# Kernel optimization log

Measured on AMD Instinct MI355X. Metric: run time of the kernel, lower is better.

## Reference

```python
import jax, jax.numpy as jnp
import numpy as np

D = 1024      # n_embd
H = 16        # n_head
HD = D // H   # head_size = 64


def _layernorm(x, g, b, eps=1e-5):
    mu = jnp.mean(x, axis=-1, keepdims=True)
    var = jnp.mean((x - mu) ** 2, axis=-1, keepdims=True)
    return (x - mu) * jax.lax.rsqrt(var + eps) * g + b


def setup_inputs() -> dict:
    key = jax.random.key(0)
    ks = jax.random.split(key, 12)
    s = lambda fan_in: 1.0 / np.sqrt(fan_in)
    inp = {
        "x": jax.random.normal(ks[0], (4, 2048, D), dtype=jnp.float32),
        # attention projections (bias=False in Head), per-head weights fused into [D, D]
        "wq": jax.random.uniform(ks[1], (D, D), jnp.float32, -s(D), s(D)),
        "wk": jax.random.uniform(ks[2], (D, D), jnp.float32, -s(D), s(D)),
        "wv": jax.random.uniform(ks[3], (D, D), jnp.float32, -s(D), s(D)),
        "wo": jax.random.uniform(ks[4], (D, D), jnp.float32, -s(D), s(D)),
        "bo": jax.random.uniform(ks[5], (D,), jnp.float32, -s(D), s(D)),
        # feed-forward: D -> 4D -> D
        "w1": jax.random.uniform(ks[6], (D, 4 * D), jnp.float32, -s(D), s(D)),
        "b1": jax.random.uniform(ks[7], (4 * D,), jnp.float32, -s(D), s(D)),
        "w2": jax.random.uniform(ks[8], (4 * D, D), jnp.float32, -s(4 * D), s(4 * D)),
        "b2": jax.random.uniform(ks[9], (D,), jnp.float32, -s(4 * D), s(4 * D)),
        # layernorms
        "g_ln1": jnp.ones((D,), jnp.float32),
        "b_ln1": jnp.zeros((D,), jnp.float32),
        "g_ln2": jnp.ones((D,), jnp.float32),
        "b_ln2": jnp.zeros((D,), jnp.float32),
    }
    return inp


def reference(x, wq, wk, wv, wo, bo, w1, b1, w2, b2, g_ln1, b_ln1, g_ln2, b_ln2):
    B, T, _ = x.shape
    # --- self-attention on ln1(x) ---
    h = _layernorm(x, g_ln1, b_ln1)
    q = (h @ wq).reshape(B, T, H, HD)
    k = (h @ wk).reshape(B, T, H, HD)
    v = (h @ wv).reshape(B, T, H, HD)
    scores = jnp.einsum("bqhd,bkhd->bhqk", q, k) * (HD ** -0.5)
    causal = jnp.tril(jnp.ones((T, T), dtype=bool))
    scores = jnp.where(causal, scores, -jnp.inf)
    wei = jax.nn.softmax(scores, axis=-1)                    # [B,H,T,T]
    attn = jnp.einsum("bhqk,bkhd->bqhd", wei, v).reshape(B, T, D)
    x = x + attn @ wo + bo
    # --- feed-forward on ln2(x) ---
    h2 = _layernorm(x, g_ln2, b_ln2)
    x = x + jax.nn.relu(h2 @ w1 + b1) @ w2 + b2
    return x
```

## Files before the change

### kernel.cpp

```cpp
#include <hip/hip_runtime.h>
#include <cstdint>

typedef __bf16 bf16x8 __attribute__((ext_vector_type(8)));
typedef float f32x4 __attribute__((ext_vector_type(4)));
typedef unsigned int u32x4 __attribute__((ext_vector_type(4)));
typedef unsigned int u32x2 __attribute__((ext_vector_type(2)));
typedef unsigned short u16x4 __attribute__((ext_vector_type(4)));

#define D_MODEL 1024
#define SEQ     2048
#define NBATCH  4
#define NHEAD   16
#define HDIM    64
#define NTOK    (NBATCH * SEQ)
#define QSCALE  0.18033688011112042f

__device__ __forceinline__ unsigned short f2bf(float f) {
  unsigned int u = __builtin_bit_cast(unsigned int, f);
  u += 0x7FFFu + ((u >> 16) & 1u);
  return (unsigned short)(u >> 16);
}

__device__ __forceinline__ float bf2f(unsigned short s) {
  return __builtin_bit_cast(float, (unsigned int)s << 16);
// ... 55 lines not shown
                                                 const float* __restrict__ bb,
                                                 unsigned short* __restrict__ out) {
  const int row = blockIdx.x, tid = threadIdx.x;
  float4 xv;
  if (FPIN) {
    xv = ((const float4*)((const float*)xin + (size_t)row * D_MODEL))[tid];
  } else {
    const u16x4 bv4 = ((const u16x4*)((const unsigned short*)xin + (size_t)row * D_MODEL))[tid];
    xv.x = bf2f(bv4.x); xv.y = bf2f(bv4.y); xv.z = bf2f(bv4.z); xv.w = bf2f(bv4.w);
  }
  float s  = xv.x + xv.y + xv.z + xv.w;
  float ss = xv.x * xv.x + xv.y * xv.y + xv.z * xv.z + xv.w * xv.w;
  #pragma unroll
  for (int off = 1; off < 64; off <<= 1) { s += __shfl_xor(s, off); ss += __shfl_xor(ss, off); }
  __shared__ float red[8];
  const int wave = tid >> 6, lane = tid & 63;
  if (lane == 0) { red[wave] = s; red[4 + wave] = ss; }
  __syncthreads();
  s  = red[0] + red[1] + red[2] + red[3];
  ss = red[4] + red[5] + red[6] + red[7];
  const float mu   = s * (1.0f / D_MODEL);
  const float var  = ss * (1.0f / D_MODEL) - mu * mu;
  const float rstd = rsqrtf(var + 1e-5f);
  const float4 gv = ((const float4*)g)[tid];
  const float4 bv = ((const float4*)bb)[tid];
  u16x4 o;
  o.x = f2bf((xv.x - mu) * rstd * gv.x + bv.x);
  o.y = f2bf((xv.y - mu) * rstd * gv.y + bv.y);
  o.z = f2bf((xv.z - mu) * rstd * gv.z + bv.z);
  o.w = f2bf((xv.w - mu) * rstd * gv.w + bv.w);
  *(u16x4*)(out + (size_t)row * D_MODEL + tid * 4) = o;
}

template <bool BIAS, bool RELU, int RES, bool OBF, bool QKV>
__global__ __launch_bounds__(256) void gemm_bt(const unsigned short* __restrict__ A,
                                               const unsigned short* __restrict__ Bt,
                                               const float* __restrict__ bias,
                                               const void* __restrict__ res,
                                               void* __restrict__ out,
                                               unsigned short* __restrict__ qb,
                                               unsigned short* __restrict__ kp,
                                               unsigned short* __restrict__ vt,
                                               int M, int N, int K) {
  __shared__ __align__(16) unsigned short As[128 * 64];
  __shared__ __align__(16) unsigned short Bs[128 * 64];
  const int tid  = threadIdx.x;
  const int lin = blockIdx.y * gridDim.x + blockIdx.x;
  const int xcd = lin & 7, idx = lin >> 3;
  const int by = xcd * 8 + (idx & 7);
  const int bx = idx >> 3;
  const int row0 = by * 128, col0 = bx * 128;
  const int wave = tid >> 6, lane = tid & 63;
  const int wm = wave >> 1, wn = wave & 1;
  const int l15 = lane & 15, quad = lane >> 4;
  f32x4 acc[4][4] = {};

  const int tr = tid >> 3;
  const int tc = (tid & 7) ^ (tr & 7);
  const unsigned short* gA = A  + (size_t)(row0 + tr) * K + tc * 8;
  const unsigned short* gB = Bt + (size_t)(col0 + tr) * K + tc * 8;

  const int rowA = (wm * 64 + l15) * 64;
  const int rowB = (wn * 64 + l15) * 64;
  const int swz0 = (quad ^ (l15 & 7)) * 8;
  const int swz1 = ((4 + quad) ^ (l15 & 7)) * 8;

  for (int k0 = 0; k0 < K; k0 += 64) {
    #pragma unroll
    for (int i = 0; i < 4; ++i) {
      gload16(gA + (size_t)(i * 32) * K + k0, As + (i * 256 + tid) * 8);
      gload16(gB + (size_t)(i * 32) * K + k0, Bs + (i * 256 + tid) * 8);
    }
    __syncthreads();
    #pragma unroll
    for (int kf = 0; kf < 2; ++kf) {
      const int swz = kf ? swz1 : swz0;
      bf16x8 af[4], bfr[4];
      #pragma unroll
      for (int t = 0; t < 4; ++t) {
        af[t]  = load8bf(As + rowA + t * 1024 + swz);
        bfr[t] = load8bf(Bs + rowB + t * 1024 + swz);
      }
      #pragma unroll
      for (int i = 0; i < 4; ++i)
        #pragma unroll
        for (int j = 0; j < 4; ++j)
          acc[i][j] = mfma16(af[i], bfr[j], acc[i][j]);
    }
    __syncthreads();
  }

  const size_t rbase = (size_t)row0 + wm * 64 + quad * 4;
  const int cbase = col0 + wn * 64 + l15;
  if (QKV) {
    const int sec = col0 >> 10;
    #pragma unroll
    for (int i = 0; i < 4; ++i) {
      #pragma unroll
      for (int j = 0; j < 4; ++j) {
        const int col = cbase + j * 16;
        if (sec == 0) {
          #pragma unroll
          for (int r = 0; r < 4; ++r) {
            const size_t row = rbase + i * 16 + r;
            qb[row * 1024 + col] = f2bf(acc[i][j][r] * QSCALE);
          }
        } else if (sec == 1) {
          const int c2 = col - 1024, hh = c2 >> 6, d = c2 & 63;
          #pragma unroll
          for (int r = 0; r < 4; ++r) {
            const size_t row = rbase + i * 16 + r;
            const int bb = (int)(row >> 11), t = (int)(row & 2047);
            kp[(((size_t)(bb * 16 + hh)) * SEQ + t) * 64 + d] = f2bf(acc[i][j][r]);
          }
        } else {
          const int c2 = col - 2048, hh = c2 >> 6, d = c2 & 63;
          const size_t t0 = rbase + i * 16;
          const int bb = (int)(t0 >> 11);
          u16x4 pk;
          #pragma unroll
          for (int r = 0; r < 4; ++r) pk[r] = f2bf(acc[i][j][r]);
          *(u16x4*)(vt + ((size_t)(bb * 16 + hh) * 64 + d) * SEQ + (t0 & 2047)) = pk;
        }
      }
    }
  } else {
    #pragma unroll
    for (int i = 0; i < 4; ++i) {
      #pragma unroll
      for (int j = 0; j < 4; ++j) {
        const int col = cbase + j * 16;
        const float bval = BIAS ? bias[col] : 0.0f;
        #pragma unroll
        for (int r = 0; r < 4; ++r) {
          const size_t row = rbase + i * 16 + r;
          float v = acc[i][j][r];
          if (BIAS) v += bval;
          if (RELU) v = fmaxf(v, 0.0f);
          if (RES == 1) v += ((const float*)res)[row * N + col];
          if (RES == 2) v += bf2f(((const unsigned short*)res)[row * N + col]);
          if (OBF)  ((unsigned short*)out)[row * N + col] = f2bf(v);
          else      ((float*)out)[row * N + col] = v;
        }
      }
    }
  }
}

__device__ __forceinline__ void stage_half_512(const unsigned short* __restrict__ src,
                                               unsigned short* dst, int K, int k0,
                                               int h, int tid) {
  #pragma unroll
  for (int l = 0; l < 2; ++l) {
    const int cid = l * 512 + tid;
    const int r = cid >> 3, p = cid & 7, c = p ^ (r & 7);
    gload16(src + (size_t)(h * 128 + r) * K + k0 + c * 8, dst + h * 8192 + cid * 8);
  }
}

template <bool BIAS, bool RELU, int RES, bool OBF, bool QKV>
__global__ __launch_bounds__(512, 2) void gemm256(const unsigned short* __restrict__ A,
                                                  const unsigned short* __restrict__ Bt,
                                                  const float* __restrict__ bias,
                                                  const void* __restrict__ res,
                                                  void* __restrict__ out,
                                                  unsigned short* __restrict__ qb,
                                                  unsigned short* __restrict__ kp,
                                                  unsigned short* __restrict__ vt,
                                                  int M, int N, int K) {
  __shared__ __align__(16) unsigned short lds[2][32768];
  const int tid = threadIdx.x;
  const int lin = blockIdx.y * gridDim.x + blockIdx.x;
  const int xcd = lin & 7, idx = lin >> 3;
  const int by = xcd * 4 + (idx & 3);
  const int bx = idx >> 2;
  const int row0 = by * 256, col0 = bx * 256;
  const int wave = tid >> 6, lane = tid & 63;
  const int wm = wave >> 2, wn = wave & 3;
  const int l15 = lane & 15, quad = lane >> 4;
  const int swz0 = (quad ^ (l15 & 7)) * 8;
  const int swz1 = ((4 + quad) ^ (l15 & 7)) * 8;

  const unsigned short* gA = A  + (size_t)row0 * K;
  const unsigned short* gB = Bt + (size_t)col0 * K;

  unsigned short* As0 = &lds[0][0];
  unsigned short* Bs0 = &lds[0][16384];
  unsigned short* As1 = &lds[1][0];
  unsigned short* Bs1 = &lds[1][16384];

  f32x4 acc[8][4] = {};
  const int KT = K >> 6;

  stage_half_512(gA, As0, K, 0, 0, tid);
  stage_half_512(gA, As0, K, 0, 1, tid);
  stage_half_512(gB, Bs0, K, 0, 0, tid);
  stage_half_512(gB, Bs0, K, 0, 1, tid);
  stage_half_512(gB, Bs1, K, 64, 0, tid);
  stage_half_512(gB, Bs1, K, 64, 1, tid);
  asm volatile("s_waitcnt vmcnt(4)" ::: "memory");
  asm volatile("s_barrier" ::: "memory");

  for (int t = 0; t < KT; ++t) {
    unsigned short* As  = (t & 1) ? As1 : As0;
    unsigned short* Bs  = (t & 1) ? Bs1 : Bs0;
    unsigned short* Asn = (t & 1) ? As0 : As1;
    const int k1 = (t + 1) << 6, k2 = (t + 2) << 6;
    bf16x8 a0[2][4], b01[2][2], b23[2][2];

    #pragma unroll
    for (int i = 0; i < 4; ++i) {
      const unsigned short* ap = As + (wm * 128 + i * 16 + l15) * 64;
      a0[0][i] = load8bf(ap + swz0);
      a0[1][i] = load8bf(ap + swz1);
    }
    #pragma unroll
    for (int j = 0; j < 2; ++j) {
      const unsigned short* bp = Bs + (wn * 64 + j * 16 + l15) * 64;
      b01[0][j] = load8bf(bp + swz0);
      b01[1][j] = load8bf(bp + swz1);
    }
    if (t + 1 < KT) stage_half_512(gA, Asn, K, k1, 0, tid);
    asm volatile("s_barrier" ::: "memory");
    __builtin_amdgcn_s_setprio(1);
    #pragma unroll
    for (int kf = 0; kf < 2; ++kf)
      #pragma unroll
      for (int i = 0; i < 4; ++i)
        #pragma unroll
        for (int j = 0; j < 2; ++j)
          acc[i][j] = mfma16(a0[kf][i], b01[kf][j], acc[i][j]);
    __builtin_amdgcn_s_setprio(0);
    asm volatile("s_barrier" ::: "memory");

    #pragma unroll
    for (int j = 0; j < 2; ++j) {
      const unsigned short* bp = Bs + (wn * 64 + 32 + j * 16 + l15) * 64;
      b23[0][j] = load8bf(bp + swz0);
      b23[1][j] = load8bf(bp + swz1);
    }
    if (t + 1 < KT) stage_half_512(gA, Asn, K, k1, 1, tid);
    asm volatile("s_barrier" ::: "memory");
    __builtin_amdgcn_s_setprio(1);
    #pragma unroll
    for (int kf = 0; kf < 2; ++kf)
      #pragma unroll
      for (int i = 0; i < 4; ++i)
        #pragma unroll
        for (int j = 0; j < 2; ++j)
          acc[i][2 + j] = mfma16(a0[kf][i], b23[kf][j], acc[i][2 + j]);
    __builtin_amdgcn_s_setprio(0);
    asm volatile("s_barrier" ::: "memory");

    #pragma unroll
    for (int i = 0; i < 4; ++i) {
      const unsigned short* ap = As + (wm * 128 + 64 + i * 16 + l15) * 64;
      a0[0][i] = load8bf(ap + swz0);
      a0[1][i] = load8bf(ap + swz1);
    }
    if (t + 2 < KT) stage_half_512(gB, Bs, K, k2, 0, tid);
    asm volatile("s_barrier" ::: "memory");
    __builtin_amdgcn_s_setprio(1);
    #pragma unroll
    for (int kf = 0; kf < 2; ++kf)
      #pragma unroll
      for (int i = 0; i < 4; ++i)
        #pragma unroll
        for (int j = 0; j < 2; ++j)
          acc[4 + i][2 + j] = mfma16(a0[kf][i], b23[kf][j], acc[4 + i][2 + j]);
    __builtin_amdgcn_s_setprio(0);
    asm volatile("s_barrier" ::: "memory");

    if (t + 2 < KT) stage_half_512(gB, Bs, K, k2, 1, tid);
    asm volatile("s_barrier" ::: "memory");
    __builtin_amdgcn_s_setprio(1);
    #pragma unroll
    for (int kf = 0; kf < 2; ++kf)
      #pragma unroll
      for (int i = 0; i < 4; ++i)
        #pragma unroll
        for (int j = 0; j < 2; ++j)
          acc[4 + i][j] = mfma16(a0[kf][i], b01[kf][j], acc[4 + i][j]);
    __builtin_amdgcn_s_setprio(0);
    if (t + 2 < KT) asm volatile("s_waitcnt vmcnt(4)" ::: "memory");
    else            asm volatile("s_waitcnt vmcnt(0)" ::: "memory");
    asm volatile("s_barrier" ::: "memory");
  }

  const size_t rbase = (size_t)row0 + wm * 128 + quad * 4;
  const int cbase = col0 + wn * 64 + l15;
  if (QKV) {
    const int sec = col0 >> 10;
    #pragma unroll
    for (int i = 0; i < 8; ++i) {
      #pragma unroll
      for (int j = 0; j < 4; ++j) {
        const int col = cbase + j * 16;
        if (sec == 0) {
          #pragma unroll
          for (int r = 0; r < 4; ++r) {
            const size_t row = rbase + i * 16 + r;
            qb[row * 1024 + col] = f2bf(acc[i][j][r] * QSCALE);
          }
        } else if (sec == 1) {
          const int c2 = col - 1024, hh = c2 >> 6, d = c2 & 63;
          #pragma unroll
          for (int r = 0; r < 4; ++r) {
            const size_t row = rbase + i * 16 + r;
            const int bb = (int)(row >> 11), tt = (int)(row & 2047);
            kp[(((size_t)(bb * 16 + hh)) * SEQ + tt) * 64 + d] = f2bf(acc[i][j][r]);
          }
        } else {
          const int c2 = col - 2048, hh = c2 >> 6, d = c2 & 63;
          const size_t t0 = rbase + i * 16;
          const int bb = (int)(t0 >> 11);
          u16x4 pk;
          #pragma unroll
          for (int r = 0; r < 4; ++r) pk[r] = f2bf(acc[i][j][r]);
          *(u16x4*)(vt + ((size_t)(bb * 16 + hh) * 64 + d) * SEQ + (t0 & 2047)) = pk;
        }
      }
    }
  } else {
    #pragma unroll
    for (int i = 0; i < 8; ++i) {
      #pragma unroll
      for (int j = 0; j < 4; ++j) {
        const int col = cbase + j * 16;
        const float bval = BIAS ? bias[col] : 0.0f;
        #pragma unroll
        for (int r = 0; r < 4; ++r) {
          const size_t row = rbase + i * 16 + r;
          float v = acc[i][j][r];
          if (BIAS) v += bval;
          if (RELU) v = fmaxf(v, 0.0f);
          if (RES == 1) v += ((const float*)res)[row * N + col];
          if (RES == 2) v += bf2f(((const unsigned short*)res)[row * N + col]);
          if (OBF)  ((unsigned short*)out)[row * N + col] = f2bf(v);
          else      ((float*)out)[row * N + col] = v;
        }
      }
    }
  }
  (void)M;
}

__global__ __launch_bounds__(256) void attn5(const unsigned short* __restrict__ qb,
                                             const unsigned short* __restrict__ kp,
                                             const unsigned short* __restrict__ vt,
                                             unsigned short* __restrict__ attnb) {
  const int lin = (blockIdx.z * 16 + blockIdx.y) * 8 + blockIdx.x;
  const int xcd = lin & 7, idx = lin >> 3;
  const int bh = xcd * 8 + (idx >> 3);
  const int xb = idx & 7;
  const int b = bh >> 4, h = bh & 15;
  const int tid = threadIdx.x, wave = tid >> 6, lane = tid & 63;
  const int l15 = lane & 15, quad = lane >> 4;
  const size_t tokbase = (size_t)b * SEQ;

  __shared__ __align__(16) unsigned short ks[64 * 64];
  __shared__ __align__(16) unsigned short vts[64 * 64];
  __shared__ __align__(16) unsigned short plds[4][32 * 64];

  const unsigned short* kbase = kp + (size_t)bh * SEQ * HDIM;
  const unsigned short* vbase = vt + (size_t)bh * HDIM * SEQ;

  for (int half = 0; half < 2; ++half) {
    const int qblk = (half == 0) ? (15 - xb) : xb;
    const int qw0 = qblk * 128 + wave * 32;

    bf16x8 qf[2][2];
    #pragma unroll
    for (int qfi = 0; qfi < 2; ++qfi)
      #pragma unroll
      for (int kf = 0; kf < 2; ++kf)
        qf[qfi][kf] = load8bf(qb + (tokbase + qw0 + qfi * 16 + l15) * 1024
                              + h * HDIM + kf * 32 + quad * 8);

    f32x4 o[2][4] = {};
// ... 93 lines not shown
                              void* d_out, int out_size, void* d_ws, size_t ws_size,
                              hipStream_t stream) {
  const float* x    = (const float*)d_in[0];
  const float* wq   = (const float*)d_in[1];
  const float* wk   = (const float*)d_in[2];
  const float* wv   = (const float*)d_in[3];
  const float* wo   = (const float*)d_in[4];
  const float* bo   = (const float*)d_in[5];
  const float* w1   = (const float*)d_in[6];
  const float* b1   = (const float*)d_in[7];
  const float* w2   = (const float*)d_in[8];
  const float* b2   = (const float*)d_in[9];
  const float* g1   = (const float*)d_in[10];
  const float* bl1  = (const float*)d_in[11];
  const float* g2   = (const float*)d_in[12];
  const float* bl2  = (const float*)d_in[13];
  float* out = (float*)d_out;

  char* ws = (char*)d_ws;
  size_t off = 0;
  auto alloc = [&](size_t bytes) { char* p = ws + off; off += (bytes + 255) & ~(size_t)255; return p; };
  unsigned short* wqkv_t = (unsigned short*)alloc((size_t)3072 * 1024 * 2);
  unsigned short* wo_t   = (unsigned short*)alloc((size_t)1024 * 1024 * 2);
  unsigned short* w1_t   = (unsigned short*)alloc((size_t)4096 * 1024 * 2);
  unsigned short* w2_t   = (unsigned short*)alloc((size_t)1024 * 4096 * 2);
  unsigned short* h1     = (unsigned short*)alloc((size_t)NTOK * 1024 * 2);
  unsigned short* kpb    = (unsigned short*)alloc((size_t)NTOK * 1024 * 2);
  unsigned short* vtb    = (unsigned short*)alloc((size_t)NTOK * 1024 * 2);
  unsigned short* attnb  = (unsigned short*)alloc((size_t)NTOK * 1024 * 2);
  unsigned short* h2     = (unsigned short*)alloc((size_t)NTOK * 1024 * 2);
  unsigned short* ffn1   = (unsigned short*)alloc((size_t)NTOK * 4096 * 2);
  unsigned short* qb  = attnb;
  unsigned short* x1b = h1;

  tcast_all<<<12288, 256, 0, stream>>>(wq, wk, wv, wo, w1, w2,
                                       wqkv_t, wo_t, w1_t, w2_t);
  ln_kernel<1><<<NTOK, 256, 0, stream>>>(x, g1, bl1, h1);
  gemm256<false, false, 0, true, true><<<dim3(12, 32), 512, 0, stream>>>(
      h1, wqkv_t, nullptr, nullptr, nullptr, qb, kpb, vtb, NTOK, 3072, 1024);
  attn5<<<dim3(SEQ / 256, NHEAD, NBATCH), 256, 0, stream>>>(qb, kpb, vtb, attnb);
  gemm_bt<true, false, 1, true, false><<<dim3(8, 64), 256, 0, stream>>>(
      attnb, wo_t, bo, x, x1b, nullptr, nullptr, nullptr, NTOK, 1024, 1024);
  ln_kernel<0><<<NTOK, 256, 0, stream>>>(x1b, g2, bl2, h2);
  gemm256<true, true, 0, true, false><<<dim3(16, 32), 512, 0, stream>>>(
      h2, w1_t, b1, nullptr, ffn1, nullptr, nullptr, nullptr, NTOK, 4096, 1024);
  gemm256<true, false, 2, false, false><<<dim3(4, 32), 512, 0, stream>>>(
      ffn1, w2_t, b2, x1b, out, nullptr, nullptr, nullptr, NTOK, 1024, 4096);
  (void)in_sizes; (void)n_in; (void)out_size; (void)ws_size;
}
```

Measured before the change: 503.8 us.

## Add 256x128-tile GEMM variant for QKV and FFN2 to raise grid occupancy

Introduces gemm256n, a 256x128 output-tile GEMM with its own double-buffered LDS schedule (A prefetched two k-steps ahead, B one step ahead). It replaces the 256x256 kernel for the QKV projection and the FFN down-projection, doubling the block count (e.g. FFN2 from 128 to 256 blocks) so more of the machine's compute units get work. The QKV-specific epilogue moves into the new kernel and is removed from the older kernels. The trade-off is lower arithmetic intensity per tile and more A-matrix traffic.

Result: faster. 447.7 us (-11.1%).

```diff
diff --git a/kernel.cpp b/kernel.cpp
--- a/kernel.cpp
+++ b/kernel.cpp
@@ -111,15 +111,12 @@
   *(u16x4*)(out + (size_t)row * D_MODEL + tid * 4) = o;
 }
 
-template <bool BIAS, bool RELU, int RES, bool OBF, bool QKV>
+template <bool BIAS, bool RELU, int RES, bool OBF>
 __global__ __launch_bounds__(256) void gemm_bt(const unsigned short* __restrict__ A,
                                                const unsigned short* __restrict__ Bt,
                                                const float* __restrict__ bias,
                                                const void* __restrict__ res,
                                                void* __restrict__ out,
-                                               unsigned short* __restrict__ qb,
-                                               unsigned short* __restrict__ kp,
-                                               unsigned short* __restrict__ vt,
                                                int M, int N, int K) {
   __shared__ __align__(16) unsigned short As[128 * 64];
   __shared__ __align__(16) unsigned short Bs[128 * 64];
@@ -171,56 +168,22 @@
 
   const size_t rbase = (size_t)row0 + wm * 64 + quad * 4;
   const int cbase = col0 + wn * 64 + l15;
-  if (QKV) {
-    const int sec = col0 >> 10;
-    #pragma unroll
-    for (int i = 0; i < 4; ++i) {
-      #pragma unroll
-      for (int j = 0; j < 4; ++j) {
-        const int col = cbase + j * 16;
-        if (sec == 0) {
-          #pragma unroll
-          for (int r = 0; r < 4; ++r) {
-            const size_t row = rbase + i * 16 + r;
-            qb[row * 1024 + col] = f2bf(acc[i][j][r] * QSCALE);
-          }
-        } else if (sec == 1) {
-          const int c2 = col - 1024, hh = c2 >> 6, d = c2 & 63;
-          #pragma unroll
-          for (int r = 0; r < 4; ++r) {
-            const size_t row = rbase + i * 16 + r;
-            const int bb = (int)(row >> 11), t = (int)(row & 2047);
-            kp[(((size_t)(bb * 16 + hh)) * SEQ + t) * 64 + d] = f2bf(acc[i][j][r]);
-          }
-        } else {
-          const int c2 = col - 2048, hh = c2 >> 6, d = c2 & 63;
-          const size_t t0 = rbase + i * 16;
-          const int bb = (int)(t0 >> 11);
-          u16x4 pk;
-          #pragma unroll
-          for (int r = 0; r < 4; ++r) pk[r] = f2bf(acc[i][j][r]);
-          *(u16x4*)(vt + ((size_t)(bb * 16 + hh) * 64 + d) * SEQ + (t0 & 2047)) = pk;
-        }
-      }
-    }
-  } else {
-    #pragma unroll
-    for (int i = 0; i < 4; ++i) {
-      #pragma unroll
-      for (int j = 0; j < 4; ++j) {
-        const int col = cbase + j * 16;
-        const float bval = BIAS ? bias[col] : 0.0f;
-        #pragma unroll
-        for (int r = 0; r < 4; ++r) {
-          const size_t row = rbase + i * 16 + r;
-          float v = acc[i][j][r];
-          if (BIAS) v += bval;
-          if (RELU) v = fmaxf(v, 0.0f);
-          if (RES == 1) v += ((const float*)res)[row * N + col];
-          if (RES == 2) v += bf2f(((const unsigned short*)res)[row * N + col]);
-          if (OBF)  ((unsigned short*)out)[row * N + col] = f2bf(v);
-          else      ((float*)out)[row * N + col] = v;
-        }
+  #pragma unroll
+  for (int i = 0; i < 4; ++i) {
+    #pragma unroll
+    for (int j = 0; j < 4; ++j) {
+      const int col = cbase + j * 16;
+      const float bval = BIAS ? bias[col] : 0.0f;
+      #pragma unroll
+      for (int r = 0; r < 4; ++r) {
+        const size_t row = rbase + i * 16 + r;
+        float v = acc[i][j][r];
+        if (BIAS) v += bval;
+        if (RELU) v = fmaxf(v, 0.0f);
+        if (RES == 1) v += ((const float*)res)[row * N + col];
+        if (RES == 2) v += bf2f(((const unsigned short*)res)[row * N + col]);
+        if (OBF)  ((unsigned short*)out)[row * N + col] = f2bf(v);
+        else      ((float*)out)[row * N + col] = v;
       }
     }
   }
@@ -237,15 +200,12 @@
   }
 }
 
-template <bool BIAS, bool RELU, int RES, bool OBF, bool QKV>
+template <bool BIAS, bool RELU, int RES, bool OBF>
 __global__ __launch_bounds__(512, 2) void gemm256(const unsigned short* __restrict__ A,
                                                   const unsigned short* __restrict__ Bt,
                                                   const float* __restrict__ bias,
                                                   const void* __restrict__ res,
                                                   void* __restrict__ out,
-                                                  unsigned short* __restrict__ qb,
-                                                  unsigned short* __restrict__ kp,
-                                                  unsigned short* __restrict__ vt,
                                                   int M, int N, int K) {
   __shared__ __align__(16) unsigned short lds[2][32768];
   const int tid = threadIdx.x;
@@ -275,9 +235,13 @@
   stage_half_512(gA, As0, K, 0, 1, tid);
   stage_half_512(gB, Bs0, K, 0, 0, tid);
   stage_half_512(gB, Bs0, K, 0, 1, tid);
-  stage_half_512(gB, Bs1, K, 64, 0, tid);
-  stage_half_512(gB, Bs1, K, 64, 1, tid);
-  asm volatile("s_waitcnt vmcnt(4)" ::: "memory");
+  if (KT > 1) {
+    stage_half_512(gB, Bs1, K, 64, 0, tid);
+    stage_half_512(gB, Bs1, K, 64, 1, tid);
+    asm volatile("s_waitcnt vmcnt(4)" ::: "memory");
+  } else {
+    asm volatile("s_waitcnt vmcnt(0)" ::: "memory");
+  }
   asm volatile("s_barrier" ::: "memory");
 
   for (int t = 0; t < KT; ++t) {
@@ -368,10 +332,137 @@
 
   const size_t rbase = (size_t)row0 + wm * 128 + quad * 4;
   const int cbase = col0 + wn * 64 + l15;
+  #pragma unroll
+  for (int i = 0; i < 8; ++i) {
+    #pragma unroll
+    for (int j = 0; j < 4; ++j) {
+      const int col = cbase + j * 16;
+      const float bval = BIAS ? bias[col] : 0.0f;
+      #pragma unroll
+      for (int r = 0; r < 4; ++r) {
+        const size_t row = rbase + i * 16 + r;
+        float v = acc[i][j][r];
+        if (BIAS) v += bval;
+        if (RELU) v = fmaxf(v, 0.0f);
+        if (RES == 1) v += ((const float*)res)[row * N + col];
+        if (RES == 2) v += bf2f(((const unsigned short*)res)[row * N + col]);
+        if (OBF)  ((unsigned short*)out)[row * N + col] = f2bf(v);
+        else      ((float*)out)[row * N + col] = v;
+      }
+    }
+  }
+  (void)M;
+}
+
+template <bool BIAS, bool RELU, int RES, bool OBF, bool QKV>
+__global__ __launch_bounds__(512, 2) void gemm256n(const unsigned short* __restrict__ A,
+                                                   const unsigned short* __restrict__ Bt,
+                                                   const float* __restrict__ bias,
+                                                   const void* __restrict__ res,
+                                                   void* __restrict__ out,
+                                                   unsigned short* __restrict__ qb,
+                                                   unsigned short* __restrict__ kp,
+                                                   unsigned short* __restrict__ vt,
+                                                   int M, int N, int K) {
+  __shared__ __align__(16) unsigned short lds[2][24576];
+  const int tid = threadIdx.x;
+  const int lin = blockIdx.y * gridDim.x + blockIdx.x;
+  const int xcd = lin & 7, idx = lin >> 3;
+  const int by = xcd * 4 + (idx & 3);
+  const int bx = idx >> 2;
+  const int row0 = by * 256, col0 = bx * 128;
+  const int wave = tid >> 6, lane = tid & 63;
+  const int wm = wave >> 1, wn = wave & 1;
+  const int l15 = lane & 15, quad = lane >> 4;
+  const int swz0 = (quad ^ (l15 & 7)) * 8;
+  const int swz1 = ((4 + quad) ^ (l15 & 7)) * 8;
+
+  const unsigned short* gA = A  + (size_t)row0 * K;
+  const unsigned short* gB = Bt + (size_t)col0 * K;
+
+  unsigned short* As0 = &lds[0][0];
+  unsigned short* Bs0 = &lds[0][16384];
+  unsigned short* As1 = &lds[1][0];
+  unsigned short* Bs1 = &lds[1][16384];
+
+  f32x4 acc[4][4] = {};
+  const int KT = K >> 6;
+
+  stage_half_512(gA, As0, K, 0, 0, tid);
+  stage_half_512(gA, As0, K, 0, 1, tid);
+  stage_half_512(gB, Bs0, K, 0, 0, tid);
+  if (KT > 1) {
+    stage_half_512(gA, As1, K, 64, 0, tid);
+    stage_half_512(gA, As1, K, 64, 1, tid);
+    asm volatile("s_waitcnt vmcnt(4)" ::: "memory");
+  } else {
+    asm volatile("s_waitcnt vmcnt(0)" ::: "memory");
+  }
+  asm volatile("s_barrier" ::: "memory");
+
+  for (int t = 0; t < KT; ++t) {
+    unsigned short* As  = (t & 1) ? As1 : As0;
+    unsigned short* Bs  = (t & 1) ? Bs1 : Bs0;
+    unsigned short* Bsn = (t & 1) ? Bs0 : Bs1;
+    const int k1 = (t + 1) << 6, k2 = (t + 2) << 6;
+    bf16x8 a0[2][4], b01[2][2], b23[2][2];
+
+    #pragma unroll
+    for (int i = 0; i < 4; ++i) {
+      const unsigned short* ap = As + (wm * 64 + i * 16 + l15) * 64;
+      a0[0][i] = load8bf(ap + swz0);
+      a0[1][i] = load8bf(ap + swz1);
+    }
+    #pragma unroll
+    for (int j = 0; j < 2; ++j) {
+      const unsigned short* bp = Bs + (wn * 64 + j * 16 + l15) * 64;
+      b01[0][j] = load8bf(bp + swz0);
+      b01[1][j] = load8bf(bp + swz1);
+    }
+    if (t + 1 < KT) stage_half_512(gB, Bsn, K, k1, 0, tid);
+    asm volatile("s_barrier" ::: "memory");
+    __builtin_amdgcn_s_setprio(1);
+    #pragma unroll
+    for (int kf = 0; kf < 2; ++kf)
+      #pragma unroll
+      for (int i = 0; i < 4; ++i)
+        #pragma unroll
+        for (int j = 0; j < 2; ++j)
+          acc[i][j] = mfma16(a0[kf][i], b01[kf][j], acc[i][j]);
+    __builtin_amdgcn_s_setprio(0);
+    asm volatile("s_barrier" ::: "memory");
+
+    #pragma unroll
+    for (int j = 0; j < 2; ++j) {
+      const unsigned short* bp = Bs + (wn * 64 + 32 + j * 16 + l15) * 64;
+      b23[0][j] = load8bf(bp + swz0);
+      b23[1][j] = load8bf(bp + swz1);
+    }
+    if (t + 2 < KT) {
+      stage_half_512(gA, As, K, k2, 0, tid);
+      stage_half_512(gA, As, K, k2, 1, tid);
+    }
+    asm volatile("s_barrier" ::: "memory");
+    __builtin_amdgcn_s_setprio(1);
+    #pragma unroll
+    for (int kf = 0; kf < 2; ++kf)
+      #pragma unroll
+      for (int i = 0; i < 4; ++i)
+        #pragma unroll
+        for (int j = 0; j < 2; ++j)
+          acc[i][2 + j] = mfma16(a0[kf][i], b23[kf][j], acc[i][2 + j]);
+    __builtin_amdgcn_s_setprio(0);
+    if (t + 2 < KT)      asm volatile("s_waitcnt vmcnt(4)" ::: "memory");
+    else if (t + 1 < KT) asm volatile("s_waitcnt vmcnt(0)" ::: "memory");
+    asm volatile("s_barrier" ::: "memory");
+  }
+
+  const size_t rbase = (size_t)row0 + wm * 64 + quad * 4;
+  const int cbase = col0 + wn * 64 + l15;
   if (QKV) {
     const int sec = col0 >> 10;
     #pragma unroll
-    for (int i = 0; i < 8; ++i) {
+    for (int i = 0; i < 4; ++i) {
       #pragma unroll
       for (int j = 0; j < 4; ++j) {
         const int col = cbase + j * 16;
@@ -402,7 +493,7 @@
     }
   } else {
     #pragma unroll
-    for (int i = 0; i < 8; ++i) {
+    for (int i = 0; i < 4; ++i) {
       #pragma unroll
       for (int j = 0; j < 4; ++j) {
         const int col = cbase + j * 16;
@@ -587,15 +678,15 @@
   tcast_all<<<12288, 256, 0, stream>>>(wq, wk, wv, wo, w1, w2,
                                        wqkv_t, wo_t, w1_t, w2_t);
   ln_kernel<1><<<NTOK, 256, 0, stream>>>(x, g1, bl1, h1);
-  gemm256<false, false, 0, true, true><<<dim3(12, 32), 512, 0, stream>>>(
+  gemm256n<false, false, 0, true, true><<<dim3(24, 32), 512, 0, stream>>>(
       h1, wqkv_t, nullptr, nullptr, nullptr, qb, kpb, vtb, NTOK, 3072, 1024);
   attn5<<<dim3(SEQ / 256, NHEAD, NBATCH), 256, 0, stream>>>(qb, kpb, vtb, attnb);
-  gemm_bt<true, false, 1, true, false><<<dim3(8, 64), 256, 0, stream>>>(
-      attnb, wo_t, bo, x, x1b, nullptr, nullptr, nullptr, NTOK, 1024, 1024);
+  gemm_bt<true, false, 1, true><<<dim3(8, 64), 256, 0, stream>>>(
+      attnb, wo_t, bo, x, x1b, NTOK, 1024, 1024);
   ln_kernel<0><<<NTOK, 256, 0, stream>>>(x1b, g2, bl2, h2);
-  gemm256<true, true, 0, true, false><<<dim3(16, 32), 512, 0, stream>>>(
-      h2, w1_t, b1, nullptr, ffn1, nullptr, nullptr, nullptr, NTOK, 4096, 1024);
-  gemm256<true, false, 2, false, false><<<dim3(4, 32), 512, 0, stream>>>(
+  gemm256<true, true, 0, true><<<dim3(16, 32), 512, 0, stream>>>(
+      h2, w1_t, b1, nullptr, ffn1, NTOK, 4096, 1024);
+  gemm256n<true, false, 2, false, false><<<dim3(8, 32), 512, 0, stream>>>(
       ffn1, w2_t, b2, x1b, out, nullptr, nullptr, nullptr, NTOK, 1024, 4096);
   (void)in_sizes; (void)n_in; (void)out_size; (void)ws_size;
 }
```

## Split FFN2 GEMM over K into two halves with separate reduce kernel

Applied to the files above, without the earlier changes.

The FFN down-projection (K=4096, only 128 tiles of 256x256) is split into two K-halves, which doubles the block count to 256 so more CUs have work. Each half writes fp32 partials into a reused workspace region. A new elementwise kernel then sums the partials and adds the bias and bf16 residual. The cost is extra fp32 partial traffic (about 64MB written and read) plus one more launch. It also removes the dead QKV path from gemm_bt and adds lda/ldb parameters so the kernel can address a slice of K.

After: 467.9 us. -7.1%, faster.

```diff
diff --git a/kernel.cpp b/kernel.cpp
--- a/kernel.cpp
+++ b/kernel.cpp
@@ -111,15 +111,12 @@
   *(u16x4*)(out + (size_t)row * D_MODEL + tid * 4) = o;
 }
 
-template <bool BIAS, bool RELU, int RES, bool OBF, bool QKV>
+template <bool BIAS, bool RELU, int RES, bool OBF>
 __global__ __launch_bounds__(256) void gemm_bt(const unsigned short* __restrict__ A,
                                                const unsigned short* __restrict__ Bt,
                                                const float* __restrict__ bias,
                                                const void* __restrict__ res,
                                                void* __restrict__ out,
-                                               unsigned short* __restrict__ qb,
-                                               unsigned short* __restrict__ kp,
-                                               unsigned short* __restrict__ vt,
                                                int M, int N, int K) {
   __shared__ __align__(16) unsigned short As[128 * 64];
   __shared__ __align__(16) unsigned short Bs[128 * 64];
@@ -171,73 +168,39 @@
 
   const size_t rbase = (size_t)row0 + wm * 64 + quad * 4;
   const int cbase = col0 + wn * 64 + l15;
-  if (QKV) {
-    const int sec = col0 >> 10;
-    #pragma unroll
-    for (int i = 0; i < 4; ++i) {
-      #pragma unroll
-      for (int j = 0; j < 4; ++j) {
-        const int col = cbase + j * 16;
-        if (sec == 0) {
-          #pragma unroll
-          for (int r = 0; r < 4; ++r) {
-            const size_t row = rbase + i * 16 + r;
-            qb[row * 1024 + col] = f2bf(acc[i][j][r] * QSCALE);
-          }
-        } else if (sec == 1) {
-          const int c2 = col - 1024, hh = c2 >> 6, d = c2 & 63;
-          #pragma unroll
-          for (int r = 0; r < 4; ++r) {
-            const size_t row = rbase + i * 16 + r;
-            const int bb = (int)(row >> 11), t = (int)(row & 2047);
-            kp[(((size_t)(bb * 16 + hh)) * SEQ + t) * 64 + d] = f2bf(acc[i][j][r]);
-          }
-        } else {
-          const int c2 = col - 2048, hh = c2 >> 6, d = c2 & 63;
-          const size_t t0 = rbase + i * 16;
-          const int bb = (int)(t0 >> 11);
-          u16x4 pk;
-          #pragma unroll
-          for (int r = 0; r < 4; ++r) pk[r] = f2bf(acc[i][j][r]);
-          *(u16x4*)(vt + ((size_t)(bb * 16 + hh) * 64 + d) * SEQ + (t0 & 2047)) = pk;
-        }
-      }
-    }
-  } else {
-    #pragma unroll
-    for (int i = 0; i < 4; ++i) {
-      #pragma unroll
-      for (int j = 0; j < 4; ++j) {
-        const int col = cbase + j * 16;
-        const float bval = BIAS ? bias[col] : 0.0f;
-        #pragma unroll
-        for (int r = 0; r < 4; ++r) {
-          const size_t row = rbase + i * 16 + r;
-          float v = acc[i][j][r];
-          if (BIAS) v += bval;
-          if (RELU) v = fmaxf(v, 0.0f);
-          if (RES == 1) v += ((const float*)res)[row * N + col];
-          if (RES == 2) v += bf2f(((const unsigned short*)res)[row * N + col]);
-          if (OBF)  ((unsigned short*)out)[row * N + col] = f2bf(v);
-          else      ((float*)out)[row * N + col] = v;
-        }
+  #pragma unroll
+  for (int i = 0; i < 4; ++i) {
+    #pragma unroll
+    for (int j = 0; j < 4; ++j) {
+      const int col = cbase + j * 16;
+      const float bval = BIAS ? bias[col] : 0.0f;
+      #pragma unroll
+      for (int r = 0; r < 4; ++r) {
+        const size_t row = rbase + i * 16 + r;
+        float v = acc[i][j][r];
+        if (BIAS) v += bval;
+        if (RELU) v = fmaxf(v, 0.0f);
+        if (RES == 1) v += ((const float*)res)[row * N + col];
+        if (RES == 2) v += bf2f(((const unsigned short*)res)[row * N + col]);
+        if (OBF)  ((unsigned short*)out)[row * N + col] = f2bf(v);
+        else      ((float*)out)[row * N + col] = v;
       }
     }
   }
 }
 
 __device__ __forceinline__ void stage_half_512(const unsigned short* __restrict__ src,
-                                               unsigned short* dst, int K, int k0,
+                                               unsigned short* dst, int ld, int k0,
                                                int h, int tid) {
   #pragma unroll
   for (int l = 0; l < 2; ++l) {
     const int cid = l * 512 + tid;
     const int r = cid >> 3, p = cid & 7, c = p ^ (r & 7);
-    gload16(src + (size_t)(h * 128 + r) * K + k0 + c * 8, dst + h * 8192 + cid * 8);
-  }
-}
-
-template <bool BIAS, bool RELU, int RES, bool OBF, bool QKV>
+    gload16(src + (size_t)(h * 128 + r) * ld + k0 + c * 8, dst + h * 8192 + cid * 8);
+  }
+}
+
+template <bool BIAS, bool RELU, int RES, bool OBF, bool QKV, bool SPLITK>
 __global__ __launch_bounds__(512, 2) void gemm256(const unsigned short* __restrict__ A,
                                                   const unsigned short* __restrict__ Bt,
                                                   const float* __restrict__ bias,
@@ -246,22 +209,25 @@
                                                   unsigned short* __restrict__ qb,
                                                   unsigned short* __restrict__ kp,
                                                   unsigned short* __restrict__ vt,
-                                                  int M, int N, int K) {
+                                                  int M, int N, int K, int lda, int ldb) {
   __shared__ __align__(16) unsigned short lds[2][32768];
   const int tid = threadIdx.x;
   const int lin = blockIdx.y * gridDim.x + blockIdx.x;
   const int xcd = lin & 7, idx = lin >> 3;
   const int by = xcd * 4 + (idx & 3);
-  const int bx = idx >> 2;
+  const int bxr = idx >> 2;
+  const int ks  = SPLITK ? (bxr >> 2) : 0;
+  const int bx  = SPLITK ? (bxr & 3) : bxr;
   const int row0 = by * 256, col0 = bx * 256;
+  const int koff = SPLITK ? ks * K : 0;
   const int wave = tid >> 6, lane = tid & 63;
   const int wm = wave >> 2, wn = wave & 3;
   const int l15 = lane & 15, quad = lane >> 4;
   const int swz0 = (quad ^ (l15 & 7)) * 8;
   const int swz1 = ((4 + quad) ^ (l15 & 7)) * 8;
 
-  const unsigned short* gA = A  + (size_t)row0 * K;
-  const unsigned short* gB = Bt + (size_t)col0 * K;
+  const unsigned short* gA = A  + (size_t)row0 * lda + koff;
+  const unsigned short* gB = Bt + (size_t)col0 * ldb + koff;
 
   unsigned short* As0 = &lds[0][0];
   unsigned short* Bs0 = &lds[0][16384];
@@ -271,13 +237,17 @@
   f32x4 acc[8][4] = {};
   const int KT = K >> 6;
 
-  stage_half_512(gA, As0, K, 0, 0, tid);
-  stage_half_512(gA, As0, K, 0, 1, tid);
-  stage_half_512(gB, Bs0, K, 0, 0, tid);
-  stage_half_512(gB, Bs0, K, 0, 1, tid);
-  stage_half_512(gB, Bs1, K, 64, 0, tid);
-  stage_half_512(gB, Bs1, K, 64, 1, tid);
-  asm volatile("s_waitcnt vmcnt(4)" ::: "memory");
+  stage_half_512(gA, As0, lda, 0, 0, tid);
+  stage_half_512(gA, As0, lda, 0, 1, tid);
+  stage_half_512(gB, Bs0, ldb, 0, 0, tid);
+  stage_half_512(gB, Bs0, ldb, 0, 1, tid);
+  if (KT > 1) {
+    stage_half_512(gB, Bs1, ldb, 64, 0, tid);
+    stage_half_512(gB, Bs1, ldb, 64, 1, tid);
+    asm volatile("s_waitcnt vmcnt(4)" ::: "memory");
+  } else {
+    asm volatile("s_waitcnt vmcnt(0)" ::: "memory");
+  }
   asm volatile("s_barrier" ::: "memory");
 
   for (int t = 0; t < KT; ++t) {
@@ -299,7 +269,7 @@
       b01[0][j] = load8bf(bp + swz0);
       b01[1][j] = load8bf(bp + swz1);
     }
-    if (t + 1 < KT) stage_half_512(gA, Asn, K, k1, 0, tid);
+    if (t + 1 < KT) stage_half_512(gA, Asn, lda, k1, 0, tid);
     asm volatile("s_barrier" ::: "memory");
     __builtin_amdgcn_s_setprio(1);
     #pragma unroll
@@ -318,7 +288,7 @@
       b23[0][j] = load8bf(bp + swz0);
       b23[1][j] = load8bf(bp + swz1);
     }
-    if (t + 1 < KT) stage_half_512(gA, Asn, K, k1, 1, tid);
+    if (t + 1 < KT) stage_half_512(gA, Asn, lda, k1, 1, tid);
     asm volatile("s_barrier" ::: "memory");
     __builtin_amdgcn_s_setprio(1);
     #pragma unroll
@@ -337,7 +307,7 @@
       a0[0][i] = load8bf(ap + swz0);
       a0[1][i] = load8bf(ap + swz1);
     }
-    if (t + 2 < KT) stage_half_512(gB, Bs, K, k2, 0, tid);
+    if (t + 2 < KT) stage_half_512(gB, Bs, ldb, k2, 0, tid);
     asm volatile("s_barrier" ::: "memory");
     __builtin_amdgcn_s_setprio(1);
     #pragma unroll
@@ -350,7 +320,7 @@
     __builtin_amdgcn_s_setprio(0);
     asm volatile("s_barrier" ::: "memory");
 
-    if (t + 2 < KT) stage_half_512(gB, Bs, K, k2, 1, tid);
+    if (t + 2 < KT) stage_half_512(gB, Bs, ldb, k2, 1, tid);
     asm volatile("s_barrier" ::: "memory");
     __builtin_amdgcn_s_setprio(1);
     #pragma unroll
@@ -400,6 +370,20 @@
         }
       }
     }
+  } else if (SPLITK) {
+    float* po = (float*)out + (size_t)ks * M * N;
+    #pragma unroll
+    for (int i = 0; i < 8; ++i) {
+      #pragma unroll
+      for (int j = 0; j < 4; ++j) {
+        const int col = cbase + j * 16;
+        #pragma unroll
+        for (int r = 0; r < 4; ++r) {
+          const size_t row = rbase + i * 16 + r;
+          po[row * N + col] = acc[i][j][r];
+        }
+      }
+    }
   } else {
     #pragma unroll
     for (int i = 0; i < 8; ++i) {
@@ -422,6 +406,24 @@
     }
   }
   (void)M;
+}
+
+__global__ __launch_bounds__(256) void ffn2_reduce(const float* __restrict__ p0,
+                                                   const float* __restrict__ p1,
+                                                   const float* __restrict__ b2,
+                                                   const unsigned short* __restrict__ x1b,
+                                                   float* __restrict__ out) {
+  const size_t i4 = (size_t)blockIdx.x * 256 + threadIdx.x;
+  const float4 a = ((const float4*)p0)[i4];
+  const float4 b = ((const float4*)p1)[i4];
+  const float4 bi = ((const float4*)b2)[i4 & 255];
+  const u16x4 rv = ((const u16x4*)x1b)[i4];
+  float4 o;
+  o.x = a.x + b.x + bi.x + bf2f(rv.x);
+  o.y = a.y + b.y + bi.y + bf2f(rv.y);
+  o.z = a.z + b.z + bi.z + bf2f(rv.z);
+  o.w = a.w + b.w + bi.w + bf2f(rv.w);
+  ((float4*)out)[i4] = o;
 }
 
 __global__ __launch_bounds__(256) void attn5(const unsigned short* __restrict__ qb,
@@ -583,19 +585,23 @@
   unsigned short* ffn1   = (unsigned short*)alloc((size_t)NTOK * 4096 * 2);
   unsigned short* qb  = attnb;
   unsigned short* x1b = h1;
+  float* part = (float*)kpb;
 
   tcast_all<<<12288, 256, 0, stream>>>(wq, wk, wv, wo, w1, w2,
                                        wqkv_t, wo_t, w1_t, w2_t);
   ln_kernel<1><<<NTOK, 256, 0, stream>>>(x, g1, bl1, h1);
-  gemm256<false, false, 0, true, true><<<dim3(12, 32), 512, 0, stream>>>(
-      h1, wqkv_t, nullptr, nullptr, nullptr, qb, kpb, vtb, NTOK, 3072, 1024);
+  gemm256<false, false, 0, true, true, false><<<dim3(12, 32), 512, 0, stream>>>(
+      h1, wqkv_t, nullptr, nullptr, nullptr, qb, kpb, vtb, NTOK, 3072, 1024, 1024, 1024);
   attn5<<<dim3(SEQ / 256, NHEAD, NBATCH), 256, 0, stream>>>(qb, kpb, vtb, attnb);
-  gemm_bt<true, false, 1, true, false><<<dim3(8, 64), 256, 0, stream>>>(
-      attnb, wo_t, bo, x, x1b, nullptr, nullptr, nullptr, NTOK, 1024, 1024);
+  gemm_bt<true, false, 1, true><<<dim3(8, 64), 256, 0, stream>>>(
+      attnb, wo_t, bo, x, x1b, NTOK, 1024, 1024);
   ln_kernel<0><<<NTOK, 256, 0, stream>>>(x1b, g2, bl2, h2);
-  gemm256<true, true, 0, true, false><<<dim3(16, 32), 512, 0, stream>>>(
-      h2, w1_t, b1, nullptr, ffn1, nullptr, nullptr, nullptr, NTOK, 4096, 1024);
-  gemm256<true, false, 2, false, false><<<dim3(4, 32), 512, 0, stream>>>(
-      ffn1, w2_t, b2, x1b, out, nullptr, nullptr, nullptr, NTOK, 1024, 4096);
+  gemm256<true, true, 0, true, false, false><<<dim3(16, 32), 512, 0, stream>>>(
+      h2, w1_t, b1, nullptr, ffn1, nullptr, nullptr, nullptr, NTOK, 4096, 1024, 1024, 1024);
+  gemm256<false, false, 0, false, false, true><<<dim3(8, 32), 512, 0, stream>>>(
+      ffn1, w2_t, nullptr, nullptr, part, nullptr, nullptr, nullptr,
+      NTOK, 1024, 2048, 4096, 4096);
+  ffn2_reduce<<<NTOK * 1024 / 4 / 256, 256, 0, stream>>>(
+      part, part + (size_t)NTOK * 1024, b2, x1b, out);
   (void)in_sizes; (void)n_in; (void)out_size; (void)ws_size;
 }
```

## Add split-K FFN2 GEMM kernel and merge barrier phases in gemm256

Applied to the files above, without the earlier changes.

Adds gemm_ffn2, a dedicated kernel for the second FFN matmul. It uses a 256x128 tile with two wave groups that each own half of K=4096, combines their partial sums through LDS, and launches twice as many blocks (256 instead of 128) so more CUs are busy. gemm256's main loop is also restructured: each half-step stages both LDS halves at once and drops the intermediate barriers, with sched_barrier added to hold instruction order. The QKV epilogue path is removed from gemm_bt. The trade-offs are extra LDS traffic for the split-K reduction and higher register pressure from issuing more loads per phase.

Result: faster. 447.3 us (-11.2%).

```diff
diff --git a/kernel.cpp b/kernel.cpp
--- a/kernel.cpp
+++ b/kernel.cpp
@@ -111,15 +111,12 @@
   *(u16x4*)(out + (size_t)row * D_MODEL + tid * 4) = o;
 }
 
-template <bool BIAS, bool RELU, int RES, bool OBF, bool QKV>
+template <bool BIAS, bool RELU, int RES, bool OBF>
 __global__ __launch_bounds__(256) void gemm_bt(const unsigned short* __restrict__ A,
                                                const unsigned short* __restrict__ Bt,
                                                const float* __restrict__ bias,
                                                const void* __restrict__ res,
                                                void* __restrict__ out,
-                                               unsigned short* __restrict__ qb,
-                                               unsigned short* __restrict__ kp,
-                                               unsigned short* __restrict__ vt,
                                                int M, int N, int K) {
   __shared__ __align__(16) unsigned short As[128 * 64];
   __shared__ __align__(16) unsigned short Bs[128 * 64];
@@ -171,69 +168,35 @@
 
   const size_t rbase = (size_t)row0 + wm * 64 + quad * 4;
   const int cbase = col0 + wn * 64 + l15;
-  if (QKV) {
-    const int sec = col0 >> 10;
-    #pragma unroll
-    for (int i = 0; i < 4; ++i) {
-      #pragma unroll
-      for (int j = 0; j < 4; ++j) {
-        const int col = cbase + j * 16;
-        if (sec == 0) {
-          #pragma unroll
-          for (int r = 0; r < 4; ++r) {
-            const size_t row = rbase + i * 16 + r;
-            qb[row * 1024 + col] = f2bf(acc[i][j][r] * QSCALE);
-          }
-        } else if (sec == 1) {
-          const int c2 = col - 1024, hh = c2 >> 6, d = c2 & 63;
-          #pragma unroll
-          for (int r = 0; r < 4; ++r) {
-            const size_t row = rbase + i * 16 + r;
-            const int bb = (int)(row >> 11), t = (int)(row & 2047);
-            kp[(((size_t)(bb * 16 + hh)) * SEQ + t) * 64 + d] = f2bf(acc[i][j][r]);
-          }
-        } else {
-          const int c2 = col - 2048, hh = c2 >> 6, d = c2 & 63;
-          const size_t t0 = rbase + i * 16;
-          const int bb = (int)(t0 >> 11);
-          u16x4 pk;
-          #pragma unroll
-          for (int r = 0; r < 4; ++r) pk[r] = f2bf(acc[i][j][r]);
-          *(u16x4*)(vt + ((size_t)(bb * 16 + hh) * 64 + d) * SEQ + (t0 & 2047)) = pk;
-        }
-      }
-    }
-  } else {
-    #pragma unroll
-    for (int i = 0; i < 4; ++i) {
-      #pragma unroll
-      for (int j = 0; j < 4; ++j) {
-        const int col = cbase + j * 16;
-        const float bval = BIAS ? bias[col] : 0.0f;
-        #pragma unroll
-        for (int r = 0; r < 4; ++r) {
-          const size_t row = rbase + i * 16 + r;
-          float v = acc[i][j][r];
-          if (BIAS) v += bval;
-          if (RELU) v = fmaxf(v, 0.0f);
-          if (RES == 1) v += ((const float*)res)[row * N + col];
-          if (RES == 2) v += bf2f(((const unsigned short*)res)[row * N + col]);
-          if (OBF)  ((unsigned short*)out)[row * N + col] = f2bf(v);
-          else      ((float*)out)[row * N + col] = v;
-        }
+  #pragma unroll
+  for (int i = 0; i < 4; ++i) {
+    #pragma unroll
+    for (int j = 0; j < 4; ++j) {
+      const int col = cbase + j * 16;
+      const float bval = BIAS ? bias[col] : 0.0f;
+      #pragma unroll
+      for (int r = 0; r < 4; ++r) {
+        const size_t row = rbase + i * 16 + r;
+        float v = acc[i][j][r];
+        if (BIAS) v += bval;
+        if (RELU) v = fmaxf(v, 0.0f);
+        if (RES == 1) v += ((const float*)res)[row * N + col];
+        if (RES == 2) v += bf2f(((const unsigned short*)res)[row * N + col]);
+        if (OBF)  ((unsigned short*)out)[row * N + col] = f2bf(v);
+        else      ((float*)out)[row * N + col] = v;
       }
     }
   }
 }
 
 __device__ __forceinline__ void stage_half_512(const unsigned short* __restrict__ src,
-                                               unsigned short* dst, int K, int k0,
+                                               unsigned short* dst, int ld, int k0,
                                                int h, int tid) {
   #pragma unroll
   for (int l = 0; l < 2; ++l) {
     const int cid = l * 512 + tid;
     const int r = cid >> 3, p = cid & 7, c = p ^ (r & 7);
-    gload16(src + (size_t)(h * 128 + r) * K + k0 + c * 8, dst + h * 8192 + cid * 8);
+    gload16(src + (size_t)(h * 128 + r) * ld + k0 + c * 8, dst + h * 8192 + cid * 8);
   }
 }
 
@@ -275,9 +238,13 @@
   stage_half_512(gA, As0, K, 0, 1, tid);
   stage_half_512(gB, Bs0, K, 0, 0, tid);
   stage_half_512(gB, Bs0, K, 0, 1, tid);
-  stage_half_512(gB, Bs1, K, 64, 0, tid);
-  stage_half_512(gB, Bs1, K, 64, 1, tid);
-  asm volatile("s_waitcnt vmcnt(4)" ::: "memory");
+  if (KT > 1) {
+    stage_half_512(gB, Bs1, K, 64, 0, tid);
+    stage_half_512(gB, Bs1, K, 64, 1, tid);
+    asm volatile("s_waitcnt vmcnt(4)" ::: "memory");
+  } else {
+    asm volatile("s_waitcnt vmcnt(0)" ::: "memory");
+  }
   asm volatile("s_barrier" ::: "memory");
 
   for (int t = 0; t < KT; ++t) {
@@ -298,9 +265,14 @@
       const unsigned short* bp = Bs + (wn * 64 + j * 16 + l15) * 64;
       b01[0][j] = load8bf(bp + swz0);
       b01[1][j] = load8bf(bp + swz1);
-    }
-    if (t + 1 < KT) stage_half_512(gA, Asn, K, k1, 0, tid);
-    asm volatile("s_barrier" ::: "memory");
+      const unsigned short* bp2 = Bs + (wn * 64 + 32 + j * 16 + l15) * 64;
+      b23[0][j] = load8bf(bp2 + swz0);
+      b23[1][j] = load8bf(bp2 + swz1);
+    }
+    if (t + 1 < KT) {
+      stage_half_512(gA, Asn, K, k1, 0, tid);
+      stage_half_512(gA, Asn, K, k1, 1, tid);
+    }
     __builtin_amdgcn_s_setprio(1);
     #pragma unroll
     for (int kf = 0; kf < 2; ++kf)
@@ -309,18 +281,6 @@
         #pragma unroll
         for (int j = 0; j < 2; ++j)
           acc[i][j] = mfma16(a0[kf][i], b01[kf][j], acc[i][j]);
-    __builtin_amdgcn_s_setprio(0);
-    asm volatile("s_barrier" ::: "memory");
-
-    #pragma unroll
-    for (int j = 0; j < 2; ++j) {
-      const unsigned short* bp = Bs + (wn * 64 + 32 + j * 16 + l15) * 64;
-      b23[0][j] = load8bf(bp + swz0);
-      b23[1][j] = load8bf(bp + swz1);
-    }
-    if (t + 1 < KT) stage_half_512(gA, Asn, K, k1, 1, tid);
-    asm volatile("s_barrier" ::: "memory");
-    __builtin_amdgcn_s_setprio(1);
     #pragma unroll
     for (int kf = 0; kf < 2; ++kf)
       #pragma unroll
@@ -329,6 +289,7 @@
         for (int j = 0; j < 2; ++j)
           acc[i][2 + j] = mfma16(a0[kf][i], b23[kf][j], acc[i][2 + j]);
     __builtin_amdgcn_s_setprio(0);
+    __builtin_amdgcn_sched_barrier(0);
     asm volatile("s_barrier" ::: "memory");
 
     #pragma unroll
@@ -337,8 +298,10 @@
       a0[0][i] = load8bf(ap + swz0);
       a0[1][i] = load8bf(ap + swz1);
     }
-    if (t + 2 < KT) stage_half_512(gB, Bs, K, k2, 0, tid);
-    asm volatile("s_barrier" ::: "memory");
+    if (t + 2 < KT) {
+      stage_half_512(gB, Bs, K, k2, 0, tid);
+      stage_half_512(gB, Bs, K, k2, 1, tid);
+    }
     __builtin_amdgcn_s_setprio(1);
     #pragma unroll
     for (int kf = 0; kf < 2; ++kf)
@@ -347,12 +310,6 @@
         #pragma unroll
         for (int j = 0; j < 2; ++j)
           acc[4 + i][2 + j] = mfma16(a0[kf][i], b23[kf][j], acc[4 + i][2 + j]);
-    __builtin_amdgcn_s_setprio(0);
-    asm volatile("s_barrier" ::: "memory");
-
-    if (t + 2 < KT) stage_half_512(gB, Bs, K, k2, 1, tid);
-    asm volatile("s_barrier" ::: "memory");
-    __builtin_amdgcn_s_setprio(1);
     #pragma unroll
     for (int kf = 0; kf < 2; ++kf)
       #pragma unroll
@@ -361,6 +318,7 @@
         for (int j = 0; j < 2; ++j)
           acc[4 + i][j] = mfma16(a0[kf][i], b01[kf][j], acc[4 + i][j]);
     __builtin_amdgcn_s_setprio(0);
+    __builtin_amdgcn_sched_barrier(0);
     if (t + 2 < KT) asm volatile("s_waitcnt vmcnt(4)" ::: "memory");
     else            asm volatile("s_waitcnt vmcnt(0)" ::: "memory");
     asm volatile("s_barrier" ::: "memory");
@@ -424,6 +382,148 @@
   (void)M;
 }
 
+__device__ __forceinline__ void stage32g(const unsigned short* __restrict__ src,
+                                         unsigned short* dst, int ld, int k0,
+                                         int h128, int t256) {
+  #pragma unroll
+  for (int l = 0; l < 2; ++l) {
+    const int cid = l * 256 + t256;
+    const int L = cid >> 3;
+    const int p = cid & 7;
+    const int c = p ^ (L & 7);
+    const int row = h128 * 128 + L * 2 + (c >> 2);
+    gload16(src + (size_t)row * ld + k0 + (c & 3) * 8, dst + h128 * 4096 + cid * 8);
+  }
+}
+
+__device__ __forceinline__ bf16x8 frag32(const unsigned short* tile, int r0,
+                                         int l15, int quad) {
+  const int row = r0 + l15;
+  const int L = row >> 1;
+  const int p = ((row & 1) * 4 + quad) ^ (L & 7);
+  return load8bf(tile + L * 64 + p * 8);
+}
+
+__global__ __launch_bounds__(512, 2) void gemm_ffn2(const unsigned short* __restrict__ A,
+                                                    const unsigned short* __restrict__ Bt,
+                                                    const float* __restrict__ bias,
+                                                    const unsigned short* __restrict__ res,
+                                                    float* __restrict__ out) {
+  __shared__ __align__(16) unsigned short lds[2][2][12288];
+  const int tid = threadIdx.x;
+  const int lin = blockIdx.y * gridDim.x + blockIdx.x;
+  const int xcd = lin & 7, idx = lin >> 3;
+  const int by = xcd * 4 + (idx & 3);
+  const int bx = idx >> 2;
+  const int row0 = by * 256, col0 = bx * 128;
+  const int wave = tid >> 6, lane = tid & 63;
+  const int ks = wave >> 2;
+  const int w4 = wave & 3;
+  const int wm = w4 >> 1, wn = w4 & 1;
+  const int l15 = lane & 15, quad = lane >> 4;
+  const int t256 = tid & 255;
+
+  const unsigned short* gA = A  + (size_t)row0 * 4096 + ks * 2048;
+  const unsigned short* gB = Bt + (size_t)col0 * 4096 + ks * 2048;
+
+  unsigned short* As0 = &lds[ks][0][0];
+  unsigned short* Bs0 = &lds[ks][0][8192];
+  unsigned short* As1 = &lds[ks][1][0];
+  unsigned short* Bs1 = &lds[ks][1][8192];
+
+  f32x4 acc[8][4] = {};
+  const int KT = 64;
+
+  stage32g(gA, As0, 4096, 0, 0, t256);
+  stage32g(gA, As0, 4096, 0, 1, t256);
+  stage32g(gB, Bs0, 4096, 0, 0, t256);
+  stage32g(gB, Bs1, 4096, 32, 0, t256);
+  asm volatile("s_waitcnt vmcnt(2)" ::: "memory");
+  asm volatile("s_barrier" ::: "memory");
+
+  for (int t = 0; t < KT; ++t) {
+    unsigned short* As  = (t & 1) ? As1 : As0;
+    unsigned short* Bs  = (t & 1) ? Bs1 : Bs0;
+    unsigned short* Asn = (t & 1) ? As0 : As1;
+    const int k1 = (t + 1) << 5, k2 = (t + 2) << 5;
+    bf16x8 a[4], b[4];
+
+    #pragma unroll
+    for (int j = 0; j < 4; ++j) b[j] = frag32(Bs, wn * 64 + j * 16, l15, quad);
+    #pragma unroll
+    for (int i = 0; i < 4; ++i) a[i] = frag32(As, wm * 128 + i * 16, l15, quad);
+    if (t + 1 < KT) {
+      stage32g(gA, Asn, 4096, k1, 0, t256);
+      stage32g(gA, Asn, 4096, k1, 1, t256);
+    }
+    __builtin_amdgcn_s_setprio(1);
+    #pragma unroll
+    for (int i = 0; i < 4; ++i)
+      #pragma unroll
+      for (int j = 0; j < 4; ++j)
+        acc[i][j] = mfma16(a[i], b[j], acc[i][j]);
+    __builtin_amdgcn_s_setprio(0);
+    __builtin_amdgcn_sched_barrier(0);
+    asm volatile("s_barrier" ::: "memory");
+
+    #pragma unroll
+    for (int i = 0; i < 4; ++i) a[i] = frag32(As, wm * 128 + 64 + i * 16, l15, quad);
+    if (t + 2 < KT) stage32g(gB, Bs, 4096, k2, 0, t256);
+    __builtin_amdgcn_s_setprio(1);
+    #pragma unroll
+    for (int i = 0; i < 4; ++i)
+      #pragma unroll
+      for (int j = 0; j < 4; ++j)
+        acc[4 + i][j] = mfma16(a[i], b[j], acc[4 + i][j]);
+    __builtin_amdgcn_s_setprio(0);
+    __builtin_amdgcn_sched_barrier(0);
+    if (t + 2 < KT) asm volatile("s_waitcnt vmcnt(2)" ::: "memory");
+    else            asm volatile("s_waitcnt vmcnt(0)" ::: "memory");
+    asm volatile("s_barrier" ::: "memory");
+  }
+
+  float* ex = (float*)&lds[0][0][0];
+  #pragma unroll
+  for (int half = 0; half < 2; ++half) {
+    __syncthreads();
+    if (ks == 1) {
+      #pragma unroll
+      for (int i = 0; i < 4; ++i)
+        #pragma unroll
+        for (int j = 0; j < 4; ++j)
+          *(f32x4*)(ex + ((size_t)(w4 * 16 + i * 4 + j)) * 256 + lane * 4) =
+              acc[half * 4 + i][j];
+    }
+    __syncthreads();
+    if (ks == 0) {
+      #pragma unroll
+      for (int i = 0; i < 4; ++i)
+        #pragma unroll
+        for (int j = 0; j < 4; ++j) {
+          const f32x4 v = *(const f32x4*)(ex + ((size_t)(w4 * 16 + i * 4 + j)) * 256 + lane * 4);
+          acc[half * 4 + i][j] += v;
+        }
+    }
+  }
+  if (ks == 0) {
+    const size_t rbase = (size_t)row0 + wm * 128 + quad * 4;
+    const int cbase = col0 + wn * 64 + l15;
+    #pragma unroll
+    for (int i = 0; i < 8; ++i) {
+      #pragma unroll
+      for (int j = 0; j < 4; ++j) {
+        const int col = cbase + j * 16;
+        const float bval = bias[col];
+        #pragma unroll
+        for (int r = 0; r < 4; ++r) {
+          const size_t row = rbase + i * 16 + r;
+          out[row * 1024 + col] = acc[i][j][r] + bval + bf2f(res[row * 1024 + col]);
+        }
+      }
+    }
+  }
+}
+
 __global__ __launch_bounds__(256) void attn5(const unsigned short* __restrict__ qb,
                                              const unsigned short* __restrict__ kp,
                                              const unsigned short* __restrict__ vt,
@@ -590,12 +690,11 @@
   gemm256<false, false, 0, true, true><<<dim3(12, 32), 512, 0, stream>>>(
       h1, wqkv_t, nullptr, nullptr, nullptr, qb, kpb, vtb, NTOK, 3072, 1024);
   attn5<<<dim3(SEQ / 256, NHEAD, NBATCH), 256, 0, stream>>>(qb, kpb, vtb, attnb);
-  gemm_bt<true, false, 1, true, false><<<dim3(8, 64), 256, 0, stream>>>(
-      attnb, wo_t, bo, x, x1b, nullptr, nullptr, nullptr, NTOK, 1024, 1024);
+  gemm_bt<true, false, 1, true><<<dim3(8, 64), 256, 0, stream>>>(
+      attnb, wo_t, bo, x, x1b, NTOK, 1024, 1024);
   ln_kernel<0><<<NTOK, 256, 0, stream>>>(x1b, g2, bl2, h2);
   gemm256<true, true, 0, true, false><<<dim3(16, 32), 512, 0, stream>>>(
       h2, w1_t, b1, nullptr, ffn1, nullptr, nullptr, nullptr, NTOK, 4096, 1024);
-  gemm256<true, false, 2, false, false><<<dim3(4, 32), 512, 0, stream>>>(
-      ffn1, w2_t, b2, x1b, out, nullptr, nullptr, nullptr, NTOK, 1024, 4096);
+  gemm_ffn2<<<dim3(8, 32), 512, 0, stream>>>(ffn1, w2_t, b2, x1b, out);
   (void)in_sizes; (void)n_in; (void)out_size; (void)ws_size;
 }
```
